# Performance work log

Hardware: AMD Instinct MI355X
Metric: run time of the kernel (lower is better)

The kernel has to match this reference:

```python
import jax, jax.numpy as jnp
import numpy as np

B, T, D_IN, H, L = 64, 512, 128, 256, 2


def setup_inputs() -> dict:
    key = jax.random.key(0)
    ks = jax.random.split(key, 5)
    s0 = 1.0 / np.sqrt(D_IN + H)  # nn.Linear default init scale (uniform bound)
    s1 = 1.0 / np.sqrt(H + H)
    return {
        "x": jax.random.normal(ks[0], (B, T, D_IN), dtype=jnp.float32),
        "W0": jax.random.uniform(ks[1], (4 * H, D_IN + H), minval=-s0, maxval=s0, dtype=jnp.float32),
        "b0": jax.random.uniform(ks[2], (4 * H,), minval=-s0, maxval=s0, dtype=jnp.float32),
        "W1": jax.random.uniform(ks[3], (4 * H, H + H), minval=-s1, maxval=s1, dtype=jnp.float32),
        "b1": jax.random.uniform(ks[4], (4 * H,), minval=-s1, maxval=s1, dtype=jnp.float32),
    }


def _lstm_layer(x_tbd, W, b):
    # x_tbd: (T, B, Din); W: (4H, Din+H); b: (4H,)
    batch = x_tbd.shape[1]
    h0 = jnp.zeros((batch, H), x_tbd.dtype)
    c0 = jnp.zeros((batch, H), x_tbd.dtype)

    def step(carry, x_t):
        h, c = carry
        # torch concat order is [h, x]
        gates = jnp.concatenate([h, x_t], axis=-1) @ W.T + b  # (B, 4H)
        f, i, o, g = jnp.split(gates, 4, axis=-1)  # chunk order: f, i, o, c_tilde
        f = jax.nn.sigmoid(f)
        i = jax.nn.sigmoid(i)
        o = jax.nn.sigmoid(o)
        g = jnp.tanh(g)
        c_new = f * c + i * g
        h_new = o * jnp.tanh(c_new)
        return (h_new, c_new), h_new

    (hT, cT), hs = jax.lax.scan(step, (h0, c0), x_tbd)
    return hs, hT, cT  # hs: (T, B, H)


def reference(x, W0, b0, W1, b1):
    x_tbd = jnp.swapaxes(x, 0, 1)  # (T, B, D)
    hs0, h0T, c0T = _lstm_layer(x_tbd, W0, b0)
    hs1, h1T, c1T = _lstm_layer(hs0, W1, b1)
    h_n = jnp.stack([h0T, h1T], axis=0)  # (L, B, H)
    c_n = jnp.stack([c0T, c1T], axis=0)
    return h1T, (h_n, c_n)
```

## Files before the change

kernel.cpp:

```cpp
#include <hip/hip_runtime.h>
#include <hip/hip_bf16.h>
#include <cstdint>

typedef unsigned int u32;
typedef unsigned short u16;
typedef __bf16 bf16x8 __attribute__((ext_vector_type(8)));
typedef float f32x4 __attribute__((ext_vector_type(4)));
typedef u16 u16x8 __attribute__((ext_vector_type(8)));

#define T_STEPS 512
#define NGRP 4
#define GQ 16
#define FLAG_STRIDE 16

#define FLAGS_BYTES (2 * NGRP * GQ * FLAG_STRIDE * 4)
#define HBUF_U32_PER_LAYER (2 * NGRP * 16 * 128)
#define HS0_OFF_BYTES (1u << 20)

__device__ __forceinline__ float sigm(float z) { return 1.f / (1.f + __expf(-z)); }
__device__ __forceinline__ float tanh_(float z) { return 1.f - 2.f / (__expf(2.f * z) + 1.f); }
__device__ __forceinline__ u16 f2bf(float f) {
    union { __bf16 b; u16 u; } v; v.b = (__bf16)f; return v.u;
}

__device__ __forceinline__ u32 gload(const u32* p) {
    return __hip_atomic_load(p, __ATOMIC_RELAXED, __HIP_MEMORY_SCOPE_AGENT);
}
__device__ __forceinline__ void gstore(u32* p, u32 v) {
    __hip_atomic_store(p, v, __ATOMIC_RELAXED, __HIP_MEMORY_SCOPE_AGENT);
}
__device__ __forceinline__ void drain_vm() {
    asm volatile("s_waitcnt vmcnt(0)" ::: "memory");
}

template <int KX, bool L0>
__device__ void lstm_body(
    int grp, int q,
    const float* __restrict__ xf,
    const float* __restrict__ W,
    const float* __restrict__ bias,
    u32* __restrict__ flags,
    u32* __restrict__ hbuf,
    u32* __restrict__ hs0,
    float* __restrict__ out,
    u16* A_lds, float* D_lds, u16* h_slice)
{
    constexpr int K = 256 + KX;
    constexpr int NHF = 8;
    constexpr int NXF = KX / 32;
    constexpr int LDA = K + 8;

    const int tid = threadIdx.x;
    const int wave = tid >> 6;
    const int lane = tid & 63;
    const int g = lane >> 4;
    const int n = lane & 15;

    const int a_gate = n >> 2;
    const int dd = n & 3;
    const int wrow = a_gate * 256 + q * 16 + (wave << 2) + dd;
    bf16x8 wfrag[K / 32];
    {
        const float* Wr = W + (long)wrow * K;
#pragma unroll
        for (int kt = 0; kt < K / 32; ++kt) {
            const float* p = Wr + kt * 32 + g * 8;
            float4 lo = *(const float4*)p;
            float4 hi = *(const float4*)(p + 4);
            bf16x8 f;
            f[0] = (__bf16)lo.x; f[1] = (__bf16)lo.y; f[2] = (__bf16)lo.z; f[3] = (__bf16)lo.w;
            f[4] = (__bf16)hi.x; f[5] = (__bf16)hi.y; f[6] = (__bf16)hi.z; f[7] = (__bf16)hi.w;
            wfrag[kt] = f;
        }
    }
    const float bias_n = bias[wrow];

    const int eb = lane & 15;
    const int edd = lane >> 4;
    const int dim_local_e = (wave << 2) + edd;
    const int bg_e = grp * 16 + eb;
    float c_state = 0.f;

    const int sb = tid >> 4;
    const int sseg = tid & 15;

    const int layer = L0 ? 0 : 1;
    u32* myflag = flags + (((layer * NGRP + grp) * GQ) + q) * FLAG_STRIDE;
    u32* poll_p = nullptr;
    int poll_delta = 0;
    bool poll_active = false;
    if (wave == 0) {
        if (L0) {
            if (lane < 16) { poll_p = flags + ((0 * NGRP + grp) * GQ + lane) * FLAG_STRIDE; poll_active = true; poll_delta = 0; }
        } else {
            if (lane < 16)      { poll_p = flags + ((0 * NGRP + grp) * GQ + lane) * FLAG_STRIDE; poll_active = true; poll_delta = 1; }
            else if (lane < 32) { poll_p = flags + ((1 * NGRP + grp) * GQ + (lane - 16)) * FLAG_STRIDE; poll_active = true; poll_delta = 0; }
        }
    }

    auto stage_x = [&](int t) {
        if constexpr (L0) {
            const float* p = xf + ((long)(grp * 16 + sb) * T_STEPS + t) * 128 + sseg * 8;
            float4 lo = *(const float4*)p;
            float4 hi = *(const float4*)(p + 4);
            u16x8 v;
            v[0] = f2bf(lo.x); v[1] = f2bf(lo.y); v[2] = f2bf(lo.z); v[3] = f2bf(lo.w);
            v[4] = f2bf(hi.x); v[5] = f2bf(hi.y); v[6] = f2bf(hi.z); v[7] = f2bf(hi.w);
            *(u16x8*)&A_lds[sb * LDA + 256 + sseg * 8] = v;
        }
    };

    bf16x8 xfrag[NXF > 0 ? NXF : 1];
    auto read_xfrags = [&] {
        if constexpr (L0) {
#pragma unroll
            for (int kt = 0; kt < NXF; ++kt)
                xfrag[kt] = __builtin_bit_cast(
                    bf16x8, *(const u16x8*)&A_lds[n * LDA + 256 + kt * 32 + g * 8]);
        }
    };

    if constexpr (L0) {
        stage_x(0);
        __syncthreads();
        read_xfrags();
    }

    bool dead = false;
    for (int s = 0; s < T_STEPS; ++s) {
        if (wave == 0) {
            const u32 tgt = (u32)(s + poll_delta);
            const bool need = poll_active && tgt > 0 && !dead;
            if (__any((int)need)) {
                int guard = 0;
                while (true) {
                    bool ok = !need || (gload(poll_p) >= tgt);
                    if (__all((int)ok)) break;
                    if (++guard > (1 << 19)) { dead = true; break; }
                }
            }
        }
        __syncthreads();

        const int rp = s & 1;
        f32x4 acc = {bias_n, bias_n, bias_n, bias_n};
        u32 hv[8];
        {
            const u32* hp = hbuf + (((size_t)rp * NGRP + grp) * 16 + sb) * 128 + sseg * 8;
#pragma unroll
            for (int j = 0; j < 8; ++j) hv[j] = gload(hp + j);
        }
        u32 xv[8];
        if constexpr (!L0) {
            const u32* xp = hs0 + (((size_t)s * 64) + grp * 16 + sb) * 128 + sseg * 8;
#pragma unroll
            for (int j = 0; j < 8; ++j) xv[j] = gload(xp + j);
        }
        if constexpr (L0) {
#pragma unroll
            for (int kt = 0; kt < NXF; ++kt)
                acc = __builtin_amdgcn_mfma_f32_16x16x32_bf16(xfrag[kt], wfrag[NHF + kt], acc, 0, 0, 0);
        }
        {
            u32* Arow = (u32*)&A_lds[sb * LDA];
#pragma unroll
            for (int j = 0; j < 8; ++j) Arow[sseg * 8 + j] = hv[j];
            if constexpr (!L0) {
#pragma unroll
                for (int j = 0; j < 8; ++j) Arow[128 + sseg * 8 + j] = xv[j];
            }
        }
        __syncthreads();

        constexpr int NLDS = L0 ? NHF : (NHF + NXF);
#pragma unroll
        for (int kt = 0; kt < NLDS; ++kt) {
            bf16x8 af = __builtin_bit_cast(
                bf16x8, *(const u16x8*)&A_lds[n * LDA + kt * 32 + g * 8]);
            acc = __builtin_amdgcn_mfma_f32_16x16x32_bf16(af, wfrag[kt], acc, 0, 0, 0);
        }

#pragma unroll
        for (int r = 0; r < 4; ++r)
            D_lds[wave * 272 + n * 17 + g * 4 + r] = acc[r];
        float ga[4];
#pragma unroll
        for (int aa = 0; aa < 4; ++aa)
            ga[aa] = D_lds[wave * 272 + (aa * 4 + edd) * 17 + eb];

        float fg = sigm(ga[0]);
        float ig = sigm(ga[1]);
        float og = sigm(ga[2]);
        float gg = tanh_(ga[3]);
        c_state = fg * c_state + ig * gg;
        float h_new = og * tanh_(c_state);
        h_slice[eb * 16 + dim_local_e] = f2bf(h_new);

        if (s == T_STEPS - 1) {
            const int o1 = bg_e * 256 + q * 16 + dim_local_e;
            if constexpr (L0) {
                out[16384 + o1] = h_new;
                out[49152 + o1] = c_state;
            } else {
                out[o1] = h_new;
                out[32768 + o1] = h_new;
                out[65536 + o1] = c_state;
            }
        }
        __syncthreads();

        const int wp = (s + 1) & 1;
        if (tid < 16) {
            const u32* hrow = (const u32*)&h_slice[tid * 16];
            u32* p = hbuf + (((size_t)wp * NGRP + grp) * 16 + tid) * 128 + q * 8;
#pragma unroll
            for (int j = 0; j < 8; ++j) gstore(p + j, hrow[j]);
        } else if (L0 && tid < 32) {
            const int b2 = tid - 16;
            const u32* hrow = (const u32*)&h_slice[b2 * 16];
            u32* p = hs0 + (((size_t)s * 64) + grp * 16 + b2) * 128 + q * 8;
#pragma unroll
            for (int j = 0; j < 8; ++j) gstore(p + j, hrow[j]);
        }
        if (wave == 0) {
            drain_vm();
            if (lane == 0) gstore(myflag, (u32)(s + 1));
        }

        if constexpr (L0) {
            if (s + 1 < T_STEPS) stage_x(s + 1);
        }
        __syncthreads();
        read_xfrags();
    }
}

__global__ __launch_bounds__(256, 1) void lstm_fused(
    const float* __restrict__ xf,
    const float* __restrict__ W0, const float* __restrict__ b0,
    const float* __restrict__ W1, const float* __restrict__ b1,
    u32* __restrict__ flags,
    u32* __restrict__ hbuf0, u32* __restrict__ hbuf1,
    u32* __restrict__ hs0,
    float* __restrict__ out)
{
    __shared__ u16 A_lds[16 * 520];
    __shared__ float D_lds[4 * 16 * 17];
    __shared__ u16 h_slice[16 * 16];

    const int bid = blockIdx.x;
    if (bid < 64) {
        lstm_body<128, true >(bid >> 4, bid & 15, xf, W0, b0, flags, hbuf0, hs0, out,
                              A_lds, D_lds, h_slice);
    } else {
        const int b2 = bid - 64;
        lstm_body<256, false>(b2 >> 4, b2 & 15, nullptr, W1, b1, flags, hbuf1, hs0, out,
                              A_lds, D_lds, h_slice);
    }
}

extern "C" void kernel_launch(void* const* d_in, const int* in_sizes, int n_in,
                              void* d_out, int out_size, void* d_ws, size_t ws_size,
                              hipStream_t stream) {
    (void)in_sizes; (void)n_in; (void)out_size;
    const float* x  = (const float*)d_in[0];
    const float* W0 = (const float*)d_in[1];
    const float* b0 = (const float*)d_in[2];
    const float* W1 = (const float*)d_in[3];
    const float* b1 = (const float*)d_in[4];
    float* out = (float*)d_out;

    char* ws = (char*)d_ws;
    u32* flags = (u32*)ws;
    u32* hbuf0 = (u32*)(ws + FLAGS_BYTES);
    u32* hbuf1 = hbuf0 + HBUF_U32_PER_LAYER;
    u32* hs0 = (u32*)(ws + HS0_OFF_BYTES);

    const size_t needed = (size_t)HS0_OFF_BYTES + (size_t)512 * 64 * 256 * 2;
    if (ws_size < needed) return;

    hipMemsetAsync(d_ws, 0, FLAGS_BYTES + (size_t)2 * HBUF_U32_PER_LAYER * 4, stream);

    lstm_fused<<<128, 256, 0, stream>>>(x, W0, b0, W1, b1, flags, hbuf0, hbuf1, hs0, out);
}
```

Baseline: 2.285 ms.

## Replace flag polling with step-tagged hidden-state rings and double-buffered LDS

Each hidden value is published as bf16 data plus a 16-bit step tag straight from the element thread into a 4-deep ring, and consumers spin on the tags of the data they need. This removes the per-step flag writes, the vmcnt drain and two of the three block barriers. Layer 1 reads layer-0 outputs from a 64-slot ring with coarse backpressure through progress counters, and the LDS A buffer is double-buffered so staging the next x can overlap. The MFMA chain is also split across four accumulators. The risks are wider spin loads, a 16-bit tag that relies on T being 512, and a larger memset of the workspace on every call.

```diff
diff --git a/kernel.cpp b/kernel.cpp
--- a/kernel.cpp
+++ b/kernel.cpp
@@ -11,26 +11,28 @@
 #define T_STEPS 512
 #define NGRP 4
 #define GQ 16
-#define FLAG_STRIDE 16
-
-#define FLAGS_BYTES (2 * NGRP * GQ * FLAG_STRIDE * 4)
-#define HBUF_U32_PER_LAYER (2 * NGRP * 16 * 128)
-#define HS0_OFF_BYTES (1u << 20)
+#define HR 4
+#define XR 64
+#define HSLOT (64 * 256)
+#define XSLOT (64 * 256)
+
+#define HBUF0_OFF (64u * 1024u)
+#define HBUF_BYTES (HR * HSLOT * 4)
+#define HBUF1_OFF (HBUF0_OFF + HBUF_BYTES)
+#define XRING_OFF (1u << 20)
+#define XRING_BYTES (XR * XSLOT * 4)
+#define WS_NEEDED (XRING_OFF + XRING_BYTES)
 
 __device__ __forceinline__ float sigm(float z) { return 1.f / (1.f + __expf(-z)); }
 __device__ __forceinline__ float tanh_(float z) { return 1.f - 2.f / (__expf(2.f * z) + 1.f); }
 __device__ __forceinline__ u16 f2bf(float f) {
     union { __bf16 b; u16 u; } v; v.b = (__bf16)f; return v.u;
 }
-
 __device__ __forceinline__ u32 gload(const u32* p) {
     return __hip_atomic_load(p, __ATOMIC_RELAXED, __HIP_MEMORY_SCOPE_AGENT);
 }
 __device__ __forceinline__ void gstore(u32* p, u32 v) {
     __hip_atomic_store(p, v, __ATOMIC_RELAXED, __HIP_MEMORY_SCOPE_AGENT);
-}
-__device__ __forceinline__ void drain_vm() {
-    asm volatile("s_waitcnt vmcnt(0)" ::: "memory");
 }
 
 template <int KX, bool L0>
@@ -39,16 +41,16 @@
     const float* __restrict__ xf,
     const float* __restrict__ W,
     const float* __restrict__ bias,
-    u32* __restrict__ flags,
-    u32* __restrict__ hbuf,
-    u32* __restrict__ hs0,
+    u32* __restrict__ prog,
+    u32* __restrict__ hring,
+    u32* __restrict__ xring,
     float* __restrict__ out,
-    u16* A_lds, float* D_lds, u16* h_slice)
+    u16* A_lds, float* D_lds)
 {
     constexpr int K = 256 + KX;
-    constexpr int NHF = 8;
-    constexpr int NXF = KX / 32;
+    constexpr int NT = K / 32;
     constexpr int LDA = K + 8;
+    constexpr int ABUF = 16 * LDA;
 
     const int tid = threadIdx.x;
     const int wave = tid >> 6;
@@ -56,14 +58,12 @@
     const int g = lane >> 4;
     const int n = lane & 15;
 
-    const int a_gate = n >> 2;
-    const int dd = n & 3;
-    const int wrow = a_gate * 256 + q * 16 + (wave << 2) + dd;
-    bf16x8 wfrag[K / 32];
+    const int wrow = (n >> 2) * 256 + q * 16 + (wave << 2) + (n & 3);
+    bf16x8 wfrag[NT];
     {
         const float* Wr = W + (long)wrow * K;
 #pragma unroll
-        for (int kt = 0; kt < K / 32; ++kt) {
+        for (int kt = 0; kt < NT; ++kt) {
             const float* p = Wr + kt * 32 + g * 8;
             float4 lo = *(const float4*)p;
             float4 hi = *(const float4*)(p + 4);
@@ -77,26 +77,16 @@
 
     const int eb = lane & 15;
     const int edd = lane >> 4;
-    const int dim_local_e = (wave << 2) + edd;
-    const int bg_e = grp * 16 + eb;
+    const int dim_local = (wave << 2) + edd;
     float c_state = 0.f;
+
+    u32* hpub = hring + ((grp * 16 + eb) * 256 + q * 16 + dim_local);
+    u32* xpub = xring + ((grp * 16 + eb) * 256 + q * 16 + dim_local);
 
     const int sb = tid >> 4;
     const int sseg = tid & 15;
-
-    const int layer = L0 ? 0 : 1;
-    u32* myflag = flags + (((layer * NGRP + grp) * GQ) + q) * FLAG_STRIDE;
-    u32* poll_p = nullptr;
-    int poll_delta = 0;
-    bool poll_active = false;
-    if (wave == 0) {
-        if (L0) {
-            if (lane < 16) { poll_p = flags + ((0 * NGRP + grp) * GQ + lane) * FLAG_STRIDE; poll_active = true; poll_delta = 0; }
-        } else {
-            if (lane < 16)      { poll_p = flags + ((0 * NGRP + grp) * GQ + lane) * FLAG_STRIDE; poll_active = true; poll_delta = 1; }
-            else if (lane < 32) { poll_p = flags + ((1 * NGRP + grp) * GQ + (lane - 16)) * FLAG_STRIDE; poll_active = true; poll_delta = 0; }
-        }
-    }
+    const u32* hcon = hring + ((grp * 16 + sb) * 256 + sseg * 16);
+    const u32* xcon = xring + ((grp * 16 + sb) * 256 + sseg * 16);
 
     auto stage_x = [&](int t) {
         if constexpr (L0) {
@@ -106,79 +96,85 @@
             u16x8 v;
             v[0] = f2bf(lo.x); v[1] = f2bf(lo.y); v[2] = f2bf(lo.z); v[3] = f2bf(lo.w);
             v[4] = f2bf(hi.x); v[5] = f2bf(hi.y); v[6] = f2bf(hi.z); v[7] = f2bf(hi.w);
-            *(u16x8*)&A_lds[sb * LDA + 256 + sseg * 8] = v;
+            *(u16x8*)&A_lds[(t & 1) * ABUF + sb * LDA + 256 + sseg * 8] = v;
         }
     };
 
-    bf16x8 xfrag[NXF > 0 ? NXF : 1];
-    auto read_xfrags = [&] {
+    stage_x(0);
+
+    for (int s = 0; s < T_STEPS; ++s) {
+        u16* Abuf = A_lds + (s & 1) * ABUF;
+        u32* Arow32 = (u32*)(Abuf + sb * LDA);
+
         if constexpr (L0) {
-#pragma unroll
-            for (int kt = 0; kt < NXF; ++kt)
-                xfrag[kt] = __builtin_bit_cast(
-                    bf16x8, *(const u16x8*)&A_lds[n * LDA + 256 + kt * 32 + g * 8]);
-        }
-    };
-
-    if constexpr (L0) {
-        stage_x(0);
-        __syncthreads();
-        read_xfrags();
-    }
-
-    bool dead = false;
-    for (int s = 0; s < T_STEPS; ++s) {
-        if (wave == 0) {
-            const u32 tgt = (u32)(s + poll_delta);
-            const bool need = poll_active && tgt > 0 && !dead;
-            if (__any((int)need)) {
-                int guard = 0;
-                while (true) {
-                    bool ok = !need || (gload(poll_p) >= tgt);
-                    if (__all((int)ok)) break;
-                    if (++guard > (1 << 19)) { dead = true; break; }
+            if ((s & 15) == 0 && s >= 48 && tid < 16) {
+                const u32 need = (u32)(s - 40);
+                const u32* pp = prog + (grp * GQ + tid) * 16;
+                int gu = 0;
+                while (gload(pp) < need && ++gu < (1 << 15)) {}
+            }
+        }
+
+        {
+            const u32* hp = hcon + (s & (HR - 1)) * HSLOT;
+            u32 wv[16];
+            if constexpr (!L0) {
+                const u32* xp = xcon + ((s + 1) & (XR - 1)) * XSLOT;
+                u32 xv[16];
+                const u32 ht = (u32)s, xt = (u32)(s + 1);
+                int gu = 0;
+                for (;;) {
+                    u32 bad = 0;
+#pragma unroll
+                    for (int j = 0; j < 16; ++j) wv[j] = gload(hp + j);
+#pragma unroll
+                    for (int j = 0; j < 16; ++j) xv[j] = gload(xp + j);
+#pragma unroll
+                    for (int j = 0; j < 16; ++j) {
+                        bad |= (wv[j] >> 16) ^ ht;
+                        bad |= (xv[j] >> 16) ^ xt;
+                    }
+                    if (!bad) break;
+                    if (++gu > (1 << 15)) break;
+                }
+#pragma unroll
+                for (int j = 0; j < 8; ++j)
+                    Arow32[128 + sseg * 8 + j] = (xv[2 * j] & 0xffffu) | (xv[2 * j + 1] << 16);
+            } else {
+                const u32 ht = (u32)s;
+                int gu = 0;
+                for (;;) {
+                    u32 bad = 0;
+#pragma unroll
+                    for (int j = 0; j < 16; ++j) wv[j] = gload(hp + j);
+#pragma unroll
+                    for (int j = 0; j < 16; ++j) bad |= (wv[j] >> 16) ^ ht;
+                    if (!bad) break;
+                    if (++gu > (1 << 15)) break;
                 }
             }
+#pragma unroll
+            for (int j = 0; j < 8; ++j)
+                Arow32[sseg * 8 + j] = (wv[2 * j] & 0xffffu) | (wv[2 * j + 1] << 16);
         }
         __syncthreads();
 
-        const int rp = s & 1;
-        f32x4 acc = {bias_n, bias_n, bias_n, bias_n};
-        u32 hv[8];
-        {
-            const u32* hp = hbuf + (((size_t)rp * NGRP + grp) * 16 + sb) * 128 + sseg * 8;
-#pragma unroll
-            for (int j = 0; j < 8; ++j) hv[j] = gload(hp + j);
-        }
-        u32 xv[8];
         if constexpr (!L0) {
-            const u32* xp = hs0 + (((size_t)s * 64) + grp * 16 + sb) * 128 + sseg * 8;
-#pragma unroll
-            for (int j = 0; j < 8; ++j) xv[j] = gload(xp + j);
-        }
-        if constexpr (L0) {
-#pragma unroll
-            for (int kt = 0; kt < NXF; ++kt)
-                acc = __builtin_amdgcn_mfma_f32_16x16x32_bf16(xfrag[kt], wfrag[NHF + kt], acc, 0, 0, 0);
-        }
-        {
-            u32* Arow = (u32*)&A_lds[sb * LDA];
-#pragma unroll
-            for (int j = 0; j < 8; ++j) Arow[sseg * 8 + j] = hv[j];
-            if constexpr (!L0) {
-#pragma unroll
-                for (int j = 0; j < 8; ++j) Arow[128 + sseg * 8 + j] = xv[j];
-            }
-        }
-        __syncthreads();
-
-        constexpr int NLDS = L0 ? NHF : (NHF + NXF);
-#pragma unroll
-        for (int kt = 0; kt < NLDS; ++kt) {
+            if (tid == 0) gstore(prog + (grp * GQ + q) * 16, (u32)(s + 1));
+        }
+
+        f32x4 a0 = {bias_n, bias_n, bias_n, bias_n};
+        f32x4 a1 = {0.f, 0.f, 0.f, 0.f}, a2 = a1, a3 = a1;
+#pragma unroll
+        for (int kt = 0; kt < NT; ++kt) {
             bf16x8 af = __builtin_bit_cast(
-                bf16x8, *(const u16x8*)&A_lds[n * LDA + kt * 32 + g * 8]);
-            acc = __builtin_amdgcn_mfma_f32_16x16x32_bf16(af, wfrag[kt], acc, 0, 0, 0);
-        }
+                bf16x8, *(const u16x8*)&Abuf[n * LDA + kt * 32 + g * 8]);
+            if ((kt & 3) == 0)      a0 = __builtin_amdgcn_mfma_f32_16x16x32_bf16(af, wfrag[kt], a0, 0, 0, 0);
+            else if ((kt & 3) == 1) a1 = __builtin_amdgcn_mfma_f32_16x16x32_bf16(af, wfrag[kt], a1, 0, 0, 0);
+            else if ((kt & 3) == 2) a2 = __builtin_amdgcn_mfma_f32_16x16x32_bf16(af, wfrag[kt], a2, 0, 0, 0);
+            else                    a3 = __builtin_amdgcn_mfma_f32_16x16x32_bf16(af, wfrag[kt], a3, 0, 0, 0);
+        }
+        f32x4 acc = (a0 + a1) + (a2 + a3);
 
 #pragma unroll
         for (int r = 0; r < 4; ++r)
@@ -194,10 +190,14 @@
         float gg = tanh_(ga[3]);
         c_state = fg * c_state + ig * gg;
         float h_new = og * tanh_(c_state);
-        h_slice[eb * 16 + dim_local_e] = f2bf(h_new);
+
+        const u32 tagged = (u32)f2bf(h_new) | ((u32)(s + 1) << 16);
+        gstore(hpub + ((s + 1) & (HR - 1)) * HSLOT, tagged);
+        if constexpr (L0)
+            gstore(xpub + ((s + 1) & (XR - 1)) * XSLOT, tagged);
 
         if (s == T_STEPS - 1) {
-            const int o1 = bg_e * 256 + q * 16 + dim_local_e;
+            const int o1 = (grp * 16 + eb) * 256 + q * 16 + dim_local;
             if constexpr (L0) {
                 out[16384 + o1] = h_new;
                 out[49152 + o1] = c_state;
@@ -207,31 +207,8 @@
                 out[65536 + o1] = c_state;
             }
         }
-        __syncthreads();
-
-        const int wp = (s + 1) & 1;
-        if (tid < 16) {
-            const u32* hrow = (const u32*)&h_slice[tid * 16];
-            u32* p = hbuf + (((size_t)wp * NGRP + grp) * 16 + tid) * 128 + q * 8;
-#pragma unroll
-            for (int j = 0; j < 8; ++j) gstore(p + j, hrow[j]);
-        } else if (L0 && tid < 32) {
-            const int b2 = tid - 16;
-            const u32* hrow = (const u32*)&h_slice[b2 * 16];
-            u32* p = hs0 + (((size_t)s * 64) + grp * 16 + b2) * 128 + q * 8;
-#pragma unroll
-            for (int j = 0; j < 8; ++j) gstore(p + j, hrow[j]);
-        }
-        if (wave == 0) {
-            drain_vm();
-            if (lane == 0) gstore(myflag, (u32)(s + 1));
-        }
-
-        if constexpr (L0) {
-            if (s + 1 < T_STEPS) stage_x(s + 1);
-        }
-        __syncthreads();
-        read_xfrags();
+
+        if (s + 1 < T_STEPS) stage_x(s + 1);
     }
 }
 
@@ -239,23 +216,22 @@
     const float* __restrict__ xf,
     const float* __restrict__ W0, const float* __restrict__ b0,
     const float* __restrict__ W1, const float* __restrict__ b1,
-    u32* __restrict__ flags,
+    u32* __restrict__ prog,
     u32* __restrict__ hbuf0, u32* __restrict__ hbuf1,
-    u32* __restrict__ hs0,
+    u32* __restrict__ xring,
     float* __restrict__ out)
 {
-    __shared__ u16 A_lds[16 * 520];
+    __shared__ u16 A_lds[2 * 16 * 520];
     __shared__ float D_lds[4 * 16 * 17];
-    __shared__ u16 h_slice[16 * 16];
 
     const int bid = blockIdx.x;
     if (bid < 64) {
-        lstm_body<128, true >(bid >> 4, bid & 15, xf, W0, b0, flags, hbuf0, hs0, out,
-                              A_lds, D_lds, h_slice);
+        lstm_body<128, true >(bid >> 4, bid & 15, xf, W0, b0, prog, hbuf0, xring, out,
+                              A_lds, D_lds);
     } else {
         const int b2 = bid - 64;
-        lstm_body<256, false>(b2 >> 4, b2 & 15, nullptr, W1, b1, flags, hbuf1, hs0, out,
-                              A_lds, D_lds, h_slice);
+        lstm_body<256, false>(b2 >> 4, b2 & 15, nullptr, W1, b1, prog, hbuf1, xring, out,
+                              A_lds, D_lds);
     }
 }
 
@@ -271,15 +247,14 @@
     float* out = (float*)d_out;
 
     char* ws = (char*)d_ws;
-    u32* flags = (u32*)ws;
-    u32* hbuf0 = (u32*)(ws + FLAGS_BYTES);
-    u32* hbuf1 = hbuf0 + HBUF_U32_PER_LAYER;
-    u32* hs0 = (u32*)(ws + HS0_OFF_BYTES);
-
-    const size_t needed = (size_t)HS0_OFF_BYTES + (size_t)512 * 64 * 256 * 2;
-    if (ws_size < needed) return;
-
-    hipMemsetAsync(d_ws, 0, FLAGS_BYTES + (size_t)2 * HBUF_U32_PER_LAYER * 4, stream);
-
-    lstm_fused<<<128, 256, 0, stream>>>(x, W0, b0, W1, b1, flags, hbuf0, hbuf1, hs0, out);
-}
+    u32* prog  = (u32*)ws;
+    u32* hbuf0 = (u32*)(ws + HBUF0_OFF);
+    u32* hbuf1 = (u32*)(ws + HBUF1_OFF);
+    u32* xring = (u32*)(ws + XRING_OFF);
+
+    if (ws_size < WS_NEEDED) return;
+
+    hipMemsetAsync(d_ws, 0, WS_NEEDED, stream);
+
+    lstm_fused<<<128, 256, 0, stream>>>(x, W0, b0, W1, b1, prog, hbuf0, hbuf1, xring, out);
+}
```

Result: slower. 3.180 ms (+39.1%).
